# Kernel tuning notes

Measured on AMD Instinct MI355X. Metric: run time of the kernel, lower is better.

Reference implementation:

```python
import jax, jax.numpy as jnp
import numpy as np

N, P, F_, E, G = 2048, 256, 512, 32768, 64  # nodes, points/node, feat_len, edges, graphs
H, D = 8, 64  # GATv2 heads, per-head dim (feat_len // 8)


def _w(k, shape, fan):
    return jax.random.normal(k, shape, jnp.float32) / np.sqrt(fan)


def setup_inputs():
    ks = jax.random.split(jax.random.key(0), 40)
    inp = {
        'pcd': jax.random.normal(ks[0], (N, P, 3), jnp.float32),
        'volume': jax.random.uniform(ks[1], (N,), jnp.float32),
        'distance': jax.random.uniform(ks[2], (N,), jnp.float32),
        'edge_count': jax.random.uniform(ks[3], (N,), jnp.float32),
        'y': (jax.random.uniform(ks[4], (N,), jnp.float32) < 0.05).astype(jnp.float32),
        # PointNet (1x1 convs == per-point matmuls, no bias)
        'pn_w1': _w(ks[5], (3, 64), 3), 'pn_w2': _w(ks[6], (64, 64), 64),
        'pn_w3': _w(ks[7], (64, 64), 64), 'pn_w4': _w(ks[8], (64, 128), 64),
        'pn_w5': _w(ks[9], (128, F_), 128),
        # MLPMultiFeature
        'mf_w1': _w(ks[10], (3, F_), 3), 'mf_b1': jnp.zeros((F_,), jnp.float32),
        'mf_w2': _w(ks[11], (2 * F_, F_), 2 * F_), 'mf_b2': jnp.zeros((F_,), jnp.float32),
        # GATv2 layer 1
        'g1_wl': _w(ks[12], (F_, F_), F_), 'g1_bl': jnp.zeros((F_,), jnp.float32),
        'g1_wr': _w(ks[13], (F_, F_), F_), 'g1_br': jnp.zeros((F_,), jnp.float32),
        'g1_att': _w(ks[14], (H, D), D), 'g1_bias': jnp.zeros((F_,), jnp.float32),
        # GATv2 layer 2
        'g2_wl': _w(ks[15], (F_, F_), F_), 'g2_bl': jnp.zeros((F_,), jnp.float32),
        'g2_wr': _w(ks[16], (F_, F_), F_), 'g2_br': jnp.zeros((F_,), jnp.float32),
        'g2_att': _w(ks[17], (H, D), D), 'g2_bias': jnp.zeros((F_,), jnp.float32),
        # classifier
        'cl_w1': _w(ks[18], (F_, 64), F_), 'cl_b1': jnp.zeros((64,), jnp.float32),
        'cl_w2': _w(ks[19], (64, 64), 64), 'cl_b2': jnp.zeros((64,), jnp.float32),
        'cl_w3': _w(ks[20], (64, 1), 64), 'cl_b3': jnp.zeros((1,), jnp.float32),
        'edge_index': jax.random.randint(ks[21], (2, E), 0, N),
        'num_graphs': G,
    }
    return inp


def _gatv2(x, src, dst, wl, bl, wr, br, att, bias, n):
    h, d = att.shape
    xl = (x @ wl + bl).reshape(n, h, d)  # source transform
    xr = (x @ wr + br).reshape(n, h, d)  # target transform
    e = jax.nn.leaky_relu(xl[src] + xr[dst], 0.2)          # [E', H, D]
    score = jnp.einsum('ehd,hd->eh', e, att)               # [E', H]
    m = jax.ops.segment_max(score, dst, num_segments=n)
    m = jnp.where(jnp.isfinite(m), m, 0.0)
    p = jnp.exp(score - m[dst])
    denom = jax.ops.segment_sum(p, dst, num_segments=n)
    alpha = p / denom[dst]                                  # segment softmax over in-edges
    out = jax.ops.segment_sum(alpha[:, :, None] * xl[src], dst, num_segments=n)
    return out.reshape(n, h * d) + bias


def _forward(pcd, volume, distance, edge_count, y,
             pn_w1, pn_w2, pn_w3, pn_w4, pn_w5,
             mf_w1, mf_b1, mf_w2, mf_b2,
             g1_wl, g1_bl, g1_wr, g1_br, g1_att, g1_bias,
             g2_wl, g2_bl, g2_wr, g2_br, g2_att, g2_bias,
             cl_w1, cl_b1, cl_w2, cl_b2, cl_w3, cl_b3,
             edge_index, num_graphs):
    n = pcd.shape[0]
    # PointNet: 1x1 convs (BN=Identity) then global max-pool over points
    hdd = jax.nn.relu(pcd @ pn_w1)
    hdd = jax.nn.relu(hdd @ pn_w2)
    hdd = jax.nn.relu(hdd @ pn_w3)
    hdd = jax.nn.relu(hdd @ pn_w4)
    hdd = jax.nn.relu(hdd @ pn_w5)
    pc_feat = hdd.max(axis=1)  # [N, F]
    # multi-feature MLP
    vd = jnp.stack([volume, distance, edge_count], axis=1)
    vdf = jax.nn.relu(vd @ mf_w1 + mf_b1)
    x = jax.nn.relu(jnp.concatenate([pc_feat, vdf], axis=1) @ mf_w2 + mf_b2)
    # GAT (GATv2Conv adds self-loops by default)
    loop = jnp.arange(n)
    src = jnp.concatenate([edge_index[0], loop])
    dst = jnp.concatenate([edge_index[1], loop])
    x = jax.nn.relu(_gatv2(x, src, dst, g1_wl, g1_bl, g1_wr, g1_br, g1_att, g1_bias, n))
    x = _gatv2(x, src, dst, g2_wl, g2_bl, g2_wr, g2_br, g2_att, g2_bias, n)
    # classifier
    hc = jax.nn.relu(x @ cl_w1 + cl_b1)
    hc = jax.nn.relu(hc @ cl_w2 + cl_b2)
    logits = (hc @ cl_w3 + cl_b3)[:, 0]
    # BCEWithLogitsLoss (mean)
    loss = jnp.mean(jnp.maximum(logits, 0.0) - logits * y + jnp.log1p(jnp.exp(-jnp.abs(logits))))
    # per-graph top1-hit; graphs are contiguous & equal-size, and the torch
    # slice logits[mask_min:mask_max] excludes the segment's last node -> [:, :-1]
    npg = n // num_graphs
    lg = logits.reshape(num_graphs, npg)[:, :-1]
    yg = y.reshape(num_graphs, npg)[:, :-1]
    hits = (jnp.argmax(lg, axis=1) == jnp.argmax(yg, axis=1)).astype(jnp.float32)
    return loss, jnp.mean(hits)


def reference(pcd, volume, distance, edge_count, y,
              pn_w1, pn_w2, pn_w3, pn_w4, pn_w5,
              mf_w1, mf_b1, mf_w2, mf_b2,
              g1_wl, g1_bl, g1_wr, g1_br, g1_att, g1_bias,
              g2_wl, g2_bl, g2_wr, g2_br, g2_att, g2_bias,
              cl_w1, cl_b1, cl_w2, cl_b2, cl_w3, cl_b3,
              edge_index, num_graphs):
    return _forward(pcd, volume, distance, edge_count, y,
                    pn_w1, pn_w2, pn_w3, pn_w4, pn_w5,
                    mf_w1, mf_b1, mf_w2, mf_b2,
                    g1_wl, g1_bl, g1_wr, g1_br, g1_att, g1_bias,
                    g2_wl, g2_bl, g2_wr, g2_br, g2_att, g2_bias,
                    cl_w1, cl_b1, cl_w2, cl_b2, cl_w3, cl_b3,
                    edge_index, num_graphs)
```

## Files before the change

### kernel.cpp

```cpp
#include <hip/hip_runtime.h>
#include <cstdint>
#include <cstddef>

#define N_NODES 2048
#define N_PTS 256
#define N_EDGE 32768
#define N_EDGE_TOT (N_EDGE + N_NODES)
#define NPG 32

typedef __attribute__((ext_vector_type(8))) short bfx8;
typedef __attribute__((ext_vector_type(4))) float f32x4;
typedef unsigned short ushort_t;

#define MFMA16(a, b, c) __builtin_amdgcn_mfma_f32_16x16x32_bf16(a, b, c, 0, 0, 0)

__device__ inline int e_src(const int* ei, int e) { return e < N_EDGE ? ei[e] : e - N_EDGE; }
__device__ inline int e_dst(const int* ei, int e) { return e < N_EDGE ? ei[N_EDGE + e] : e - N_EDGE; }

__device__ inline ushort_t bf16_rtne(float v) {
  unsigned u = __float_as_uint(v);
  return (ushort_t)((u + 0x7fffu + ((u >> 16) & 1u)) >> 16);
}
__device__ inline void split2(float v, ushort_t& h, ushort_t& l) {
  h = bf16_rtne(v);
  float hf = __uint_as_float(((unsigned)h) << 16);
  l = bf16_rtne(v - hf);
}

__device__ inline unsigned cvtpk_bf16(float a, float b) {
  unsigned r;
  asm("v_cvt_pk_bf16_f32 %0, %1, %2" : "=v"(r) : "v"(a), "v"(b));
  return r;
}
__device__ inline void split2pk(float a, float b, unsigned& hp, unsigned& lp) {
  hp = cvtpk_bf16(a, b);
  float ha = __uint_as_float(hp << 16);
  float hb = __uint_as_float(hp & 0xffff0000u);
  lp = cvtpk_bf16(a - ha, b - hb);
}

__global__ void k_hist(const int* __restrict__ ei, int* __restrict__ cnt) {
  int e = blockIdx.x * 256 + threadIdx.x;
  if (e >= N_EDGE_TOT) return;
  atomicAdd(&cnt[e_dst(ei, e)], 1);
}

__global__ __launch_bounds__(256) void k_scan(int* __restrict__ cnt, int* __restrict__ row_ptr) {
  __shared__ int sS[256];
  const int t = threadIdx.x;
  int v[8]; int s = 0;
#pragma unroll
  for (int i = 0; i < 8; i++) { v[i] = cnt[t * 8 + i]; s += v[i]; }
#pragma unroll
  for (int i = 0; i < 8; i++) cnt[t * 8 + i] = 0;
  sS[t] = s;
  __syncthreads();
  for (int off = 1; off < 256; off <<= 1) {
    int x = 0;
    if (t >= off) x = sS[t - off];
    __syncthreads();
    sS[t] += x;
    __syncthreads();
  }
  int run = sS[t] - s;
#pragma unroll
  for (int i = 0; i < 8; i++) { row_ptr[t * 8 + i] = run; run += v[i]; }
  if (t == 255) row_ptr[2048] = run;
}

__global__ void k_scatter(const int* __restrict__ ei, const int* __restrict__ row_ptr,
                          int* __restrict__ cur, int* __restrict__ edge_list) {
  int e = blockIdx.x * 256 + threadIdx.x;
  if (e >= N_EDGE_TOT) return;
  int d = e_dst(ei, e);
  int pos = row_ptr[d] + atomicAdd(&cur[d], 1);
  edge_list[pos] = e;
}

__device__ inline void split_tile(const float* __restrict__ src, ushort_t* __restrict__ dh,
                                  ushort_t* __restrict__ dl, int K, int N,
                                  int k0, int n0, int t) {
  __shared__ float sT[64][65];
  const int lr = t >> 4, lc = (t & 15) * 4;
#pragma unroll
  for (int p = 0; p < 4; p++) {
    int k = lr + p * 16;
    float4 v = *(const float4*)(src + (size_t)(k0 + k) * N + n0 + lc);
    sT[k][lc] = v.x; sT[k][lc + 1] = v.y; sT[k][lc + 2] = v.z; sT[k][lc + 3] = v.w;
  }
  __syncthreads();
  const int wr = t >> 4, wc = (t & 15) * 4;
#pragma unroll
  for (int p = 0; p < 4; p++) {
    int nrow = wr + p * 16;
    uint2 uh, ul;
    split2pk(sT[wc + 0][nrow], sT[wc + 1][nrow], uh.x, ul.x);
    split2pk(sT[wc + 2][nrow], sT[wc + 3][nrow], uh.y, ul.y);
    *(uint2*)(dh + (size_t)(n0 + nrow) * K + k0 + wc) = uh;
    *(uint2*)(dl + (size_t)(n0 + nrow) * K + k0 + wc) = ul;
  }
}

__global__ __launch_bounds__(256) void k_split(const float* __restrict__ src,
                                               ushort_t* __restrict__ dh,
                                               ushort_t* __restrict__ dl, int K, int N) {
  split_tile(src, dh, dl, K, N, blockIdx.x * 64, blockIdx.y * 64, threadIdx.x);
}

__global__ __launch_bounds__(256) void k_split4(const float* __restrict__ s0,
                                                const float* __restrict__ s1,
                                                const float* __restrict__ s2,
                                                const float* __restrict__ s3,
                                                ushort_t* __restrict__ base) {
  const int z = blockIdx.z;
  const float* src = (z == 0) ? s0 : (z == 1) ? s1 : (z == 2) ? s2 : s3;
  ushort_t* dh = base + (size_t)(z >> 1) * 1048576 + (size_t)(z & 1) * 262144;
  ushort_t* dl = dh + 524288;
  split_tile(src, dh, dl, 512, 512, blockIdx.x * 64, blockIdx.y * 64, threadIdx.x);
}

constexpr size_t U_W2H = 0,       U_W2L = 4096;
constexpr size_t U_W3H = 8192,    U_W3L = 12288;
constexpr size_t U_W4H = 16384,   U_W4L = 24576;
constexpr size_t U_W5H = 32768,   U_W5L = 98304;
constexpr size_t U_MFH = 163840,  U_MFL = 688128;
constexpr size_t U_G1H = 1212416;
constexpr size_t U_G1L = 1736704;
constexpr size_t U_G2H = 2260992;
constexpr size_t U_G2L = 2785280;
constexpr size_t U_CL1H = 3309568, U_CL1L = 3342336;
constexpr size_t U_END  = 3375104;

__global__ __launch_bounds__(256) void k_splitPN(const float* __restrict__ w2,
                                                 const float* __restrict__ w3,
                                                 const float* __restrict__ w4,
                                                 const float* __restrict__ w5,
                                                 ushort_t* __restrict__ ush) {
  const int z = blockIdx.x;
  const float* src; ushort_t* dh; ushort_t* dl; int K, N, k0, n0;
  if (z == 0)      { src = w2; dh = ush + U_W2H; dl = ush + U_W2L; K = 64;  N = 64;  k0 = 0; n0 = 0; }
  else if (z == 1) { src = w3; dh = ush + U_W3H; dl = ush + U_W3L; K = 64;  N = 64;  k0 = 0; n0 = 0; }
  else if (z < 4)  { src = w4; dh = ush + U_W4H; dl = ush + U_W4L; K = 64;  N = 128; k0 = 0; n0 = (z - 2) * 64; }
  else { int i = z - 4; src = w5; dh = ush + U_W5H; dl = ush + U_W5L; K = 128; N = 512;
         k0 = (i >> 3) * 64; n0 = (i & 7) * 64; }
  split_tile(src, dh, dl, K, N, k0, n0, threadIdx.x);
}

__global__ __launch_bounds__(512, 2) void k_pointnet(
    const float* __restrict__ pcd, const float* __restrict__ w1,
    const ushort_t* __restrict__ w2th, const ushort_t* __restrict__ w2tl,
    const ushort_t* __restrict__ w3th, const ushort_t* __restrict__ w3tl,
    const ushort_t* __restrict__ w4th, const ushort_t* __restrict__ w4tl,
    const ushort_t* __restrict__ w5th, const ushort_t* __restrict__ w5tl,
    float* __restrict__ xcat) {
  __shared__ ushort_t sH4H[256 * 128];
  __shared__ ushort_t sH4L[256 * 128];
  __shared__ ushort_t sBAH[32 * 64];
  __shared__ ushort_t sBAL[32 * 64];
  __shared__ ushort_t sBBH[32 * 64];
  __shared__ ushort_t sBBL[32 * 64];
  __shared__ float sP[256 * 3];
  __shared__ float sW1[3 * 64];

  char* H4H = (char*)sH4H; char* H4L = (char*)sH4L;
  char* BAH = (char*)sBAH; char* BAL = (char*)sBAL;
  char* BBH = (char*)sBBH; char* BBL = (char*)sBBL;

  const int t = threadIdx.x;
  const int node = blockIdx.x;
  const int w = t >> 6;
  const int lane = t & 63;
  const int l15 = lane & 15;
  const int kg = lane >> 4;

  for (int i = t; i < 768; i += 512) sP[i] = pcd[(size_t)node * 768 + i];
  for (int i = t; i < 192; i += 512) sW1[i] = w1[i];

  const int rt14 = w >> 2;
  const int ct14 = w & 3;
  bfx8 b2h[2], b2l[2], b3h[2], b3l[2], b4h[2][2], b4l[2][2];
#pragma unroll
  for (int ks = 0; ks < 2; ks++) {
    {
      int col = ct14 * 16 + l15;
      int k = ks * 32 + kg * 8;
      b2h[ks] = *(const bfx8*)(w2th + col * 64 + k);
      b2l[ks] = *(const bfx8*)(w2tl + col * 64 + k);
      b3h[ks] = *(const bfx8*)(w3th + col * 64 + k);
      b3l[ks] = *(const bfx8*)(w3tl + col * 64 + k);
    }
#pragma unroll
    for (int u = 0; u < 2; u++) {
      int col = (ct14 * 2 + u) * 16 + l15;
      int k = ks * 32 + kg * 8;
      b4h[u][ks] = *(const bfx8*)(w4th + col * 64 + k);
      b4l[u][ks] = *(const bfx8*)(w4tl + col * 64 + k);
    }
  }
  __syncthreads();

  const int l1r = t >> 4, l1c = t & 15;

  {
    const float* p = &sP[(0 * 32 + l1r) * 3];
    float p0 = p[0], p1 = p[1], p2 = p[2];
    float vv[4];
#pragma unroll
    for (int j = 0; j < 4; j++) {
      int col = l1c * 4 + j;
      vv[j] = fmaxf(fmaf(p0, sW1[col], fmaf(p1, sW1[64 + col], p2 * sW1[128 + col])), 0.0f);
    }
    unsigned hp0, lp0, hp1, lp1;
    split2pk(vv[0], vv[1], hp0, lp0);
    split2pk(vv[2], vv[3], hp1, lp1);
    int off = (l1r * 128 + l1c * 8) ^ ((l1r & 7) << 4);
    *(unsigned*)(BAH + off) = hp0;
    *(unsigned*)(BAH + off + 4) = hp1;
    *(unsigned*)(BAL + off) = lp0;
    *(unsigned*)(BAL + off + 4) = lp1;
  }
  __syncthreads();

  for (int c = 0; c < 8; c++) {
    char* Ah = (c & 1) ? BBH : BAH;
    char* Al = (c & 1) ? BBL : BAL;
    char* Bh = (c & 1) ? BAH : BBH;
    char* Bl = (c & 1) ? BAL : BBL;
    {
      f32x4 acc = {0.f, 0.f, 0.f, 0.f};
#pragma unroll
      for (int ks = 0; ks < 2; ks++) {
        int row = rt14 * 16 + l15;
        int k0 = ks * 32 + kg * 8;
        int offb = (row * 128 + k0 * 2) ^ ((row & 7) << 4);
        bfx8 ah = *(const bfx8*)(Ah + offb);
        bfx8 al = *(const bfx8*)(Al + offb);
        acc = MFMA16(ah, b2h[ks], acc);
        acc = MFMA16(al, b2h[ks], acc);
        acc = MFMA16(ah, b2l[ks], acc);
      }
      unsigned hp[2], lp[2];
      split2pk(fmaxf(acc[0], 0.f), fmaxf(acc[1], 0.f), hp[0], lp[0]);
      split2pk(fmaxf(acc[2], 0.f), fmaxf(acc[3], 0.f), hp[1], lp[1]);
      const int colb = (ct14 * 16 + l15) * 2;
      const int rowb = rt14 * 16 + kg * 4;
#pragma unroll
      for (int j = 0; j < 4; j++) {
        int row = rowb + j;
        int off = (row * 128 + colb) ^ ((row & 7) << 4);
        *(ushort_t*)(Bh + off) = (ushort_t)(hp[j >> 1] >> ((j & 1) * 16));
        *(ushort_t*)(Bl + off) = (ushort_t)(lp[j >> 1] >> ((j & 1) * 16));
      }
    }
    __syncthreads();
    {
      f32x4 acc = {0.f, 0.f, 0.f, 0.f};
#pragma unroll
      for (int ks = 0; ks < 2; ks++) {
        int row = rt14 * 16 + l15;
        int k0 = ks * 32 + kg * 8;
        int offb = (row * 128 + k0 * 2) ^ ((row & 7) << 4);
        bfx8 ah = *(const bfx8*)(Bh + offb);
        bfx8 al = *(const bfx8*)(Bl + offb);
        acc = MFMA16(ah, b3h[ks], acc);
        acc = MFMA16(al, b3h[ks], acc);
        acc = MFMA16(ah, b3l[ks], acc);
      }
      unsigned hp[2], lp[2];
      split2pk(fmaxf(acc[0], 0.f), fmaxf(acc[1], 0.f), hp[0], lp[0]);
      split2pk(fmaxf(acc[2], 0.f), fmaxf(acc[3], 0.f), hp[1], lp[1]);
      const int colb = (ct14 * 16 + l15) * 2;
      const int rowb = rt14 * 16 + kg * 4;
#pragma unroll
      for (int j = 0; j < 4; j++) {
        int row = rowb + j;
        int off = (row * 128 + colb) ^ ((row & 7) << 4);
        *(ushort_t*)(Ah + off) = (ushort_t)(hp[j >> 1] >> ((j & 1) * 16));
        *(ushort_t*)(Al + off) = (ushort_t)(lp[j >> 1] >> ((j & 1) * 16));
      }
    }
    __syncthreads();
    {
      f32x4 acc[2];
      acc[0] = (f32x4){0.f, 0.f, 0.f, 0.f};
      acc[1] = (f32x4){0.f, 0.f, 0.f, 0.f};
#pragma unroll
      for (int ks = 0; ks < 2; ks++) {
        int row = rt14 * 16 + l15;
        int k0 = ks * 32 + kg * 8;
        int offb = (row * 128 + k0 * 2) ^ ((row & 7) << 4);
        bfx8 ah = *(const bfx8*)(Ah + offb);
        bfx8 al = *(const bfx8*)(Al + offb);
#pragma unroll
        for (int u = 0; u < 2; u++) {
          acc[u] = MFMA16(ah, b4h[u][ks], acc[u]);
          acc[u] = MFMA16(al, b4h[u][ks], acc[u]);
          acc[u] = MFMA16(ah, b4l[u][ks], acc[u]);
        }
      }
      if (c < 7) {
        const float* p = &sP[((c + 1) * 32 + l1r) * 3];
        float p0 = p[0], p1 = p[1], p2 = p[2];
        float vv[4];
#pragma unroll
        for (int j = 0; j < 4; j++) {
          int col = l1c * 4 + j;
          vv[j] = fmaxf(fmaf(p0, sW1[col], fmaf(p1, sW1[64 + col], p2 * sW1[128 + col])), 0.0f);
        }
        unsigned hp0, lp0, hp1, lp1;
        split2pk(vv[0], vv[1], hp0, lp0);
        split2pk(vv[2], vv[3], hp1, lp1);
        int off = (l1r * 128 + l1c * 8) ^ ((l1r & 7) << 4);
        *(unsigned*)(Bh + off) = hp0;
        *(unsigned*)(Bh + off + 4) = hp1;
        *(unsigned*)(Bl + off) = lp0;
        *(unsigned*)(Bl + off + 4) = lp1;
      }
#pragma unroll
      for (int j = 0; j < 4; j++) {
        unsigned hp, lp;
        split2pk(fmaxf(acc[0][j], 0.f), fmaxf(acc[1][j], 0.f), hp, lp);
        int row = c * 32 + rt14 * 16 + kg * 4 + j;
        int col0 = (ct14 * 2) * 16 + l15;
        int off0 = (row * 256 + col0 * 2) ^ ((row & 7) << 4);
        int off1 = ((row * 256 + (col0 + 16) * 2)) ^ ((row & 7) << 4);
        *(ushort_t*)(H4H + off0) = (ushort_t)hp;
        *(ushort_t*)(H4H + off1) = (ushort_t)(hp >> 16);
        *(ushort_t*)(H4L + off0) = (ushort_t)lp;
        *(ushort_t*)(H4L + off1) = (ushort_t)(lp >> 16);
      }
    }
    __syncthreads();
  }

  __builtin_amdgcn_sched_barrier(0);
  bfx8 b5h[4][4], b5l[4][4];
  const int c0 = w * 64;
#pragma unroll
  for (int ks = 0; ks < 4; ks++)
#pragma unroll
    for (int ct = 0; ct < 4; ct++) {
      int col = c0 + ct * 16 + l15;
      int k = ks * 32 + kg * 8;
      b5h[ks][ct] = *(const bfx8*)(w5th + col * 128 + k);
      b5l[ks][ct] = *(const bfx8*)(w5tl + col * 128 + k);
    }
  float runmax[4] = {0.f, 0.f, 0.f, 0.f};
  for (int rc = 0; rc < 8; rc++) {
    f32x4 acc[2][4];
#pragma unroll
    for (int rt = 0; rt < 2; rt++)
#pragma unroll
      for (int ct = 0; ct < 4; ct++) acc[rt][ct] = (f32x4){0.f, 0.f, 0.f, 0.f};
#pragma unroll
    for (int ks = 0; ks < 4; ks++) {
      bfx8 ah[2], al[2];
#pragma unroll
      for (int rt = 0; rt < 2; rt++) {
        int row = rc * 32 + rt * 16 + l15;
        int k0 = ks * 32 + kg * 8;
        int off = (row * 256 + k0 * 2) ^ ((row & 7) << 4);
        ah[rt] = *(const bfx8*)(H4H + off);
        al[rt] = *(const bfx8*)(H4L + off);
      }
#pragma unroll
      for (int ct = 0; ct < 4; ct++)
#pragma unroll
        for (int rt = 0; rt < 2; rt++) {
          acc[rt][ct] = MFMA16(ah[rt], b5h[ks][ct], acc[rt][ct]);
          acc[rt][ct] = MFMA16(al[rt], b5h[ks][ct], acc[rt][ct]);
          acc[rt][ct] = MFMA16(ah[rt], b5l[ks][ct], acc[rt][ct]);
        }
    }
#pragma unroll
    for (int ct = 0; ct < 4; ct++)
#pragma unroll
      for (int rt = 0; rt < 2; rt++)
#pragma unroll
        for (int j = 0; j < 4; j++)
          runmax[ct] = fmaxf(runmax[ct], acc[rt][ct][j]);
  }
#pragma unroll
  for (int ct = 0; ct < 4; ct++) {
    float m = runmax[ct];
    m = fmaxf(m, __shfl_xor(m, 16));
    m = fmaxf(m, __shfl_xor(m, 32));
    if (lane < 16) xcat[(size_t)node * 1024 + c0 + ct * 16 + lane] = m;
  }
}

__global__ void k_vdf(const float* __restrict__ vol, const float* __restrict__ dist,
                      const float* __restrict__ ec, const float* __restrict__ w1,
                      const float* __restrict__ b1, float* __restrict__ xcat) {
  int idx = blockIdx.x * 256 + threadIdx.x;
  int n = idx >> 9, j = idx & 511;
  float v = vol[n] * w1[j] + dist[n] * w1[512 + j] + ec[n] * w1[1024 + j] + b1[j];
  xcat[(size_t)n * 1024 + 512 + j] = fmaxf(v, 0.0f);
}

template <int ACT>
__global__ __launch_bounds__(256) void k_mgemm(const float* __restrict__ A,
                                               const ushort_t* __restrict__ Bh,
                                               const ushort_t* __restrict__ Bl,
                                               const float* __restrict__ bias,
                                               const float* __restrict__ bias2,
                                               float* __restrict__ C,
                                               int M, int N, int K) {
  __shared__ ushort_t sAh[4096], sAl[4096], sBh[4096], sBl[4096];
  char* pAh = (char*)sAh; char* pAl = (char*)sAl;
  char* pBh = (char*)sBh; char* pBl = (char*)sBl;
  const int t = threadIdx.x;
  const int w = t >> 6, lane = t & 63, l15 = lane & 15, kg = lane >> 4;
  const int row0 = blockIdx.x * 64, col0 = blockIdx.y * 64;
  const int sr = t >> 2;
  const int sc = (t & 3) * 16;
  const int sswz = (sr & 7) << 4;
  const int sbase = sr * 128 + sc * 2;
  f32x4 acc[4];
#pragma unroll
  for (int ct = 0; ct < 4; ct++) acc[ct] = (f32x4){0.f, 0.f, 0.f, 0.f};

  for (int kb = 0; kb < K; kb += 64) {
    __syncthreads();
    {
      const float* Ap = A + (size_t)(row0 + sr) * K + kb + sc;
      float4 a0 = *(const float4*)(Ap);
      float4 a1 = *(const float4*)(Ap + 4);
      float4 a2 = *(const float4*)(Ap + 8);
      float4 a3 = *(const float4*)(Ap + 12);
      union { bfx8 v; unsigned u[4]; } vh0, vh1, vl0, vl1;
      split2pk(a0.x, a0.y, vh0.u[0], vl0.u[0]);
      split2pk(a0.z, a0.w, vh0.u[1], vl0.u[1]);
      split2pk(a1.x, a1.y, vh0.u[2], vl0.u[2]);
      split2pk(a1.z, a1.w, vh0.u[3], vl0.u[3]);
      split2pk(a2.x, a2.y, vh1.u[0], vl1.u[0]);
      split2pk(a2.z, a2.w, vh1.u[1], vl1.u[1]);
      split2pk(a3.x, a3.y, vh1.u[2], vl1.u[2]);
      split2pk(a3.z, a3.w, vh1.u[3], vl1.u[3]);
      *(bfx8*)(pAh + ((sbase) ^ sswz)) = vh0.v;
      *(bfx8*)(pAh + ((sbase + 16) ^ sswz)) = vh1.v;
      *(bfx8*)(pAl + ((sbase) ^ sswz)) = vl0.v;
      *(bfx8*)(pAl + ((sbase + 16) ^ sswz)) = vl1.v;
    }
    {
      const ushort_t* Bph = Bh + (size_t)(col0 + sr) * K + kb + sc;
      const ushort_t* Bpl = Bl + (size_t)(col0 + sr) * K + kb + sc;
      bfx8 b0 = *(const bfx8*)Bph, b1 = *(const bfx8*)(Bph + 8);
      bfx8 c0v = *(const bfx8*)Bpl, c1v = *(const bfx8*)(Bpl + 8);
      *(bfx8*)(pBh + ((sbase) ^ sswz)) = b0;
      *(bfx8*)(pBh + ((sbase + 16) ^ sswz)) = b1;
      *(bfx8*)(pBl + ((sbase) ^ sswz)) = c0v;
      *(bfx8*)(pBl + ((sbase + 16) ^ sswz)) = c1v;
    }
    __syncthreads();
#pragma unroll
    for (int ks = 0; ks < 2; ks++) {
      const int arow = w * 16 + l15;
      const int k2 = (ks * 32 + kg * 8) * 2;
      const int aoff = (arow * 128 + k2) ^ ((arow & 7) << 4);
      bfx8 ah = *(const bfx8*)(pAh + aoff);
      bfx8 al = *(const bfx8*)(pAl + aoff);
#pragma unroll
      for (int ct = 0; ct < 4; ct++) {
        const int bcol = ct * 16 + l15;
        const int boff = (bcol * 128 + k2) ^ ((bcol & 7) << 4);
        bfx8 bh = *(const bfx8*)(pBh + boff);
        bfx8 bl = *(const bfx8*)(pBl + boff);
        acc[ct] = MFMA16(ah, bh, acc[ct]);
        acc[ct] = MFMA16(al, bh, acc[ct]);
        acc[ct] = MFMA16(ah, bl, acc[ct]);
      }
    }
  }
#pragma unroll
  for (int ct = 0; ct < 4; ct++)
#pragma unroll
    for (int j = 0; j < 4; j++) {
      int r = row0 + w * 16 + kg * 4 + j;
      int cc = col0 + ct * 16 + l15;
      float b = (cc < 512) ? bias[cc] : bias2[cc - 512];
      float v = acc[ct][j] + b;
      if (ACT == 1) v = fmaxf(v, 0.0f);
      C[(size_t)r * N + cc] = v;
    }
}

__global__ __launch_bounds__(256) void k_mgemm_mf(const float* __restrict__ A,
                                                  const float* __restrict__ vol,
                                                  const float* __restrict__ dist,
                                                  const float* __restrict__ ec,
                                                  const float* __restrict__ w1,
                                                  const float* __restrict__ b1,
                                                  const ushort_t* __restrict__ Bh,
                                                  const ushort_t* __restrict__ Bl,
                                                  const float* __restrict__ bias,
                                                  float* __restrict__ C) {
  const int M = 2048, N = 512, K = 1024;
  __shared__ ushort_t sAh[4096], sAl[4096], sBh[4096], sBl[4096];
  char* pAh = (char*)sAh; char* pAl = (char*)sAl;
  char* pBh = (char*)sBh; char* pBl = (char*)sBl;
  const int t = threadIdx.x;
  const int w = t >> 6, lane = t & 63, l15 = lane & 15, kg = lane >> 4;
  const int row0 = blockIdx.x * 64, col0 = blockIdx.y * 64;
  const int sr = t >> 2;
  const int sc = (t & 3) * 16;
  const int sswz = (sr & 7) << 4;
  const int sbase = sr * 128 + sc * 2;
  f32x4 acc[4];
#pragma unroll
  for (int ct = 0; ct < 4; ct++) acc[ct] = (f32x4){0.f, 0.f, 0.f, 0.f};

  const int r = row0 + sr;
  const float v0 = vol[r], d0 = dist[r], e0 = ec[r];

  for (int kb = 0; kb < K; kb += 64) {
    __syncthreads();
    {
      const int kc = kb + sc;
      float4 a0, a1, a2, a3;
      if (kc < 512) {
        const float* Ap = A + (size_t)r * 1024 + kc;
        a0 = *(const float4*)(Ap);
        a1 = *(const float4*)(Ap + 4);
        a2 = *(const float4*)(Ap + 8);
        a3 = *(const float4*)(Ap + 12);
      } else {
        const int j = kc - 512;
        float tmp[16];
#pragma unroll
        for (int i = 0; i < 16; i++) {
          float v = v0 * w1[j + i] + d0 * w1[512 + j + i] + e0 * w1[1024 + j + i] + b1[j + i];
          tmp[i] = fmaxf(v, 0.0f);
        }
        a0 = make_float4(tmp[0], tmp[1], tmp[2], tmp[3]);
        a1 = make_float4(tmp[4], tmp[5], tmp[6], tmp[7]);
        a2 = make_float4(tmp[8], tmp[9], tmp[10], tmp[11]);
        a3 = make_float4(tmp[12], tmp[13], tmp[14], tmp[15]);
      }
      union { bfx8 v; unsigned u[4]; } vh0, vh1, vl0, vl1;
      split2pk(a0.x, a0.y, vh0.u[0], vl0.u[0]);
      split2pk(a0.z, a0.w, vh0.u[1], vl0.u[1]);
      split2pk(a1.x, a1.y, vh0.u[2], vl0.u[2]);
      split2pk(a1.z, a1.w, vh0.u[3], vl0.u[3]);
      split2pk(a2.x, a2.y, vh1.u[0], vl1.u[0]);
      split2pk(a2.z, a2.w, vh1.u[1], vl1.u[1]);
      split2pk(a3.x, a3.y, vh1.u[2], vl1.u[2]);
      split2pk(a3.z, a3.w, vh1.u[3], vl1.u[3]);
      *(bfx8*)(pAh + ((sbase) ^ sswz)) = vh0.v;
      *(bfx8*)(pAh + ((sbase + 16) ^ sswz)) = vh1.v;
      *(bfx8*)(pAl + ((sbase) ^ sswz)) = vl0.v;
      *(bfx8*)(pAl + ((sbase + 16) ^ sswz)) = vl1.v;
    }
    {
      const ushort_t* Bph = Bh + (size_t)(col0 + sr) * K + kb + sc;
      const ushort_t* Bpl = Bl + (size_t)(col0 + sr) * K + kb + sc;
      bfx8 b0 = *(const bfx8*)Bph, b1v = *(const bfx8*)(Bph + 8);
      bfx8 c0v = *(const bfx8*)Bpl, c1v = *(const bfx8*)(Bpl + 8);
      *(bfx8*)(pBh + ((sbase) ^ sswz)) = b0;
      *(bfx8*)(pBh + ((sbase + 16) ^ sswz)) = b1v;
      *(bfx8*)(pBl + ((sbase) ^ sswz)) = c0v;
      *(bfx8*)(pBl + ((sbase + 16) ^ sswz)) = c1v;
    }
    __syncthreads();
#pragma unroll
    for (int ks = 0; ks < 2; ks++) {
      const int arow = w * 16 + l15;
      const int k2 = (ks * 32 + kg * 8) * 2;
      const int aoff = (arow * 128 + k2) ^ ((arow & 7) << 4);
      bfx8 ah = *(const bfx8*)(pAh + aoff);
      bfx8 al = *(const bfx8*)(pAl + aoff);
#pragma unroll
      for (int ct = 0; ct < 4; ct++) {
        const int bcol = ct * 16 + l15;
        const int boff = (bcol * 128 + k2) ^ ((bcol & 7) << 4);
        bfx8 bh = *(const bfx8*)(pBh + boff);
        bfx8 bl = *(const bfx8*)(pBl + boff);
        acc[ct] = MFMA16(ah, bh, acc[ct]);
        acc[ct] = MFMA16(al, bh, acc[ct]);
        acc[ct] = MFMA16(ah, bl, acc[ct]);
      }
    }
  }
#pragma unroll
  for (int ct = 0; ct < 4; ct++)
#pragma unroll
    for (int j = 0; j < 4; j++) {
      int rr = row0 + w * 16 + kg * 4 + j;
      int cc = col0 + ct * 16 + l15;
      float v = acc[ct][j] + bias[cc];
      C[(size_t)rr * N + cc] = fmaxf(v, 0.0f);
    }
}

template <int ACT>
__global__ __launch_bounds__(256) void k_gemm(const float* __restrict__ A,
                                              const float* __restrict__ W,
                                              const float* __restrict__ bias,
                                              float* __restrict__ C, int M, int N, int K,
                                              int ldc, int cof) {
  __shared__ float sA[64][17];
  __shared__ float sW[16][64];
  const int t = threadIdx.x;
  const int row0 = blockIdx.x * 64, col0 = blockIdx.y * 64;
  const int tr = t >> 4, tc = t & 15;
  const int la_r = t >> 2, la_c = (t & 3) * 4;
  const int lw_r = t >> 4, lw_c = (t & 15) * 4;
  float acc[4][4] = {};
  for (int kb = 0; kb < K; kb += 16) {
    __syncthreads();
    float4 av = *(const float4*)(A + (size_t)(row0 + la_r) * K + kb + la_c);
    sA[la_r][la_c + 0] = av.x; sA[la_r][la_c + 1] = av.y;
    sA[la_r][la_c + 2] = av.z; sA[la_r][la_c + 3] = av.w;
    float4 wv = *(const float4*)(W + (size_t)(kb + lw_r) * N + col0 + lw_c);
    *(float4*)&sW[lw_r][lw_c] = wv;
    __syncthreads();
#pragma unroll
    for (int kk = 0; kk < 16; kk++) {
      float a0 = sA[tr * 4 + 0][kk], a1 = sA[tr * 4 + 1][kk];
      float a2 = sA[tr * 4 + 2][kk], a3 = sA[tr * 4 + 3][kk];
      float4 w4 = *(const float4*)&sW[kk][tc * 4];
      acc[0][0] = fmaf(a0, w4.x, acc[0][0]); acc[0][1] = fmaf(a0, w4.y, acc[0][1]);
      acc[0][2] = fmaf(a0, w4.z, acc[0][2]); acc[0][3] = fmaf(a0, w4.w, acc[0][3]);
      acc[1][0] = fmaf(a1, w4.x, acc[1][0]); acc[1][1] = fmaf(a1, w4.y, acc[1][1]);
      acc[1][2] = fmaf(a1, w4.z, acc[1][2]); acc[1][3] = fmaf(a1, w4.w, acc[1][3]);
      acc[2][0] = fmaf(a2, w4.x, acc[2][0]); acc[2][1] = fmaf(a2, w4.y, acc[2][1]);
      acc[2][2] = fmaf(a2, w4.z, acc[2][2]); acc[2][3] = fmaf(a2, w4.w, acc[2][3]);
      acc[3][0] = fmaf(a3, w4.x, acc[3][0]); acc[3][1] = fmaf(a3, w4.y, acc[3][1]);
      acc[3][2] = fmaf(a3, w4.z, acc[3][2]); acc[3][3] = fmaf(a3, w4.w, acc[3][3]);
    }
  }
#pragma unroll
  for (int i = 0; i < 4; i++) {
    int r = row0 + tr * 4 + i;
#pragma unroll
    for (int j = 0; j < 4; j++) {
      int c = col0 + tc * 4 + j;
      float v = acc[i][j] + bias[c];
      if (ACT == 1) v = fmaxf(v, 0.0f);
      C[(size_t)r * ldc + cof + c] = v;
    }
  }
}

template <int ACT>
__global__ __launch_bounds__(256) void k_gat(
    const float* __restrict__ xlr, const float* __restrict__ att,
    const int* __restrict__ row_ptr, const int* __restrict__ edge_list,
    const int* __restrict__ ei, const float* __restrict__ bias,
    float* __restrict__ out) {
  __shared__ float sXr[512];
  __shared__ float sPb[32][8];
  __shared__ int sSrc[32];
  __shared__ float sM[8], sD[8], sScale[8];
  const int n = blockIdx.x, t = threadIdx.x;
  const int wv = t >> 6, l = t & 63;
  float attr[8];
#pragma unroll
  for (int h = 0; h < 8; h++) attr[h] = att[h * 64 + l];
  for (int i = t; i < 512; i += 256) sXr[i] = xlr[(size_t)n * 1024 + 512 + i];
  if (t < 8) { sM[t] = -1e30f; sD[t] = 0.f; }
  const int f0 = t, f1 = t + 256;
  const int h0 = f0 >> 6, h1 = f1 >> 6;
  float acc0 = 0.f, acc1 = 0.f;
  const int beg = row_ptr[n], end = row_ptr[n + 1];
  __syncthreads();
  for (int b = beg; b < end; b += 32) {
    const int cnt = min(32, end - b);
    for (int i = wv; i < cnt; i += 4) {
      const int e = edge_list[b + i];
      const int s = e_src(ei, e);
      const float* xs = xlr + (size_t)s * 1024;
      float ps[8];
#pragma unroll
      for (int h = 0; h < 8; h++) {
        float v = xs[h * 64 + l] + sXr[h * 64 + l];
        v = v > 0.f ? v : 0.2f * v;
        ps[h] = v * attr[h];
      }
#pragma unroll
      for (int off = 1; off < 64; off <<= 1)
#pragma unroll
        for (int h = 0; h < 8; h++) ps[h] += __shfl_xor(ps[h], off);
      if (l == 0) {
        sSrc[i] = s;
#pragma unroll
        for (int h = 0; h < 8; h++) sPb[i][h] = ps[h];
      }
    }
    __syncthreads();
    if (t < 8) {
      float m = sM[t];
      for (int i = 0; i < cnt; i++) m = fmaxf(m, sPb[i][t]);
      float scale = expf(sM[t] - m);
      float d = sD[t] * scale;
      for (int i = 0; i < cnt; i++) {
        float p = expf(sPb[i][t] - m);
        sPb[i][t] = p;
        d += p;
      }
      sM[t] = m; sD[t] = d; sScale[t] = scale;
    }
    __syncthreads();
    acc0 *= sScale[h0];
    acc1 *= sScale[h1];
    for (int i = 0; i < cnt; i++) {
      const float* xs = xlr + (size_t)sSrc[i] * 1024;
      acc0 = fmaf(sPb[i][h0], xs[f0], acc0);
      acc1 = fmaf(sPb[i][h1], xs[f1], acc1);
    }
    __syncthreads();
  }
  float v0 = acc0 / sD[h0] + bias[f0];
  float v1 = acc1 / sD[h1] + bias[f1];
  if (ACT == 1) { v0 = fmaxf(v0, 0.f); v1 = fmaxf(v1, 0.f); }
  out[(size_t)n * 512 + f0] = v0;
  out[(size_t)n * 512 + f1] = v1;
}

__global__ __launch_bounds__(1024) void k_final(const float* __restrict__ hc2,
                                                const float* __restrict__ w3,
                                                const float* __restrict__ b3,
                                                const float* __restrict__ y,
                                                float* __restrict__ out) {
  __shared__ float sL[2048];
  __shared__ float sRed[1024];
  __shared__ float sW[64];
  const int t = threadIdx.x;
  if (t < 64) sW[t] = w3[t];
  __syncthreads();
  float lp = 0.0f;
  for (int n = t; n < 2048; n += 1024) {
    const float4* r = (const float4*)(hc2 + (size_t)n * 64);
    float a = 0.0f;
#pragma unroll
    for (int k = 0; k < 16; k++) {
      float4 v = r[k];
      a += v.x * sW[4 * k] + v.y * sW[4 * k + 1] + v.z * sW[4 * k + 2] + v.w * sW[4 * k + 3];
    }
    a += b3[0];
    sL[n] = a;
    lp += fmaxf(a, 0.0f) - a * y[n] + log1pf(expf(-fabsf(a)));
  }
  sRed[t] = lp;
  __syncthreads();
  for (int off = 512; off > 0; off >>= 1) {
    if (t < off) sRed[t] += sRed[t + off];
    __syncthreads();
  }
  if (t == 0) out[0] = sRed[0] * (1.0f / 2048.0f);
  __syncthreads();
  float hit = 0.0f;
  if (t < 64) {
    const int base = t * NPG;
    float bl = sL[base]; int bi = 0;
    float by = y[base];  int byi = 0;
    for (int i = 1; i < NPG - 1; i++) {
      float v = sL[base + i];
      if (v > bl) { bl = v; bi = i; }
      float w = y[base + i];
      if (w > by) { by = w; byi = i; }
    }
    hit = (bi == byi) ? 1.0f : 0.0f;
  }
  __syncthreads();
  sRed[t] = hit;
  __syncthreads();
  for (int off = 512; off > 0; off >>= 1) {
    if (t < off) sRed[t] += sRed[t + off];
    __syncthreads();
  }
  if (t == 0) out[1] = sRed[0] * (1.0f / 64.0f);
}

constexpr size_t OFF_XCAT = 0;
constexpr size_t OFF_X1   = OFF_XCAT + (size_t)2048 * 1024;
constexpr size_t OFF_XL   = OFF_X1 + (size_t)2048 * 512;
constexpr size_t OFF_XR   = OFF_XL + (size_t)2048 * 512;
constexpr size_t OFF_G1   = OFF_XR + (size_t)2048 * 512;
constexpr size_t OFF_G2   = OFF_G1 + (size_t)2048 * 512;
constexpr size_t OFF_HC1  = OFF_G2 + (size_t)2048 * 512;
constexpr size_t OFF_HC2  = OFF_HC1 + (size_t)2048 * 64;
constexpr size_t OFF_SC   = OFF_HC2 + (size_t)2048 * 64;
constexpr size_t OFF_P    = OFF_SC + (size_t)N_EDGE_TOT * 8;
constexpr size_t OFF_M    = OFF_P + (size_t)N_EDGE_TOT * 8;
constexpr size_t OFF_DEN  = OFF_M + (size_t)2048 * 8;
constexpr size_t OFF_RP   = OFF_DEN + (size_t)2048 * 8;
constexpr size_t OFF_CNT  = OFF_RP + 2052;
constexpr size_t OFF_EL   = OFF_CNT + 2048;
constexpr size_t OFF_USH  = OFF_EL + 34816;

constexpr size_t WS_NEED_FULL = (OFF_USH + (U_END + 1) / 2) * sizeof(float);

extern "C" void kernel_launch(void* const* d_in, const int* in_sizes, int n_in,
                              void* d_out, int out_size, void* d_ws, size_t ws_size,
                              hipStream_t stream) {
  const float* pcd   = (const float*)d_in[0];
  const float* vol   = (const float*)d_in[1];
  const float* dist  = (const float*)d_in[2];
  const float* ecnt  = (const float*)d_in[3];
  const float* y     = (const float*)d_in[4];
  const float* pn_w1 = (const float*)d_in[5];
  const float* pn_w2 = (const float*)d_in[6];
  const float* pn_w3 = (const float*)d_in[7];
  const float* pn_w4 = (const float*)d_in[8];
  const float* pn_w5 = (const float*)d_in[9];
  const float* mf_w1 = (const float*)d_in[10];
  const float* mf_b1 = (const float*)d_in[11];
  const float* mf_w2 = (const float*)d_in[12];
  const float* mf_b2 = (const float*)d_in[13];
  const float* g1_wl = (const float*)d_in[14];
  const float* g1_bl = (const float*)d_in[15];
  const float* g1_wr = (const float*)d_in[16];
  const float* g1_br = (const float*)d_in[17];
  const float* g1_at = (const float*)d_in[18];
  const float* g1_bi = (const float*)d_in[19];
  const float* g2_wl = (const float*)d_in[20];
  const float* g2_bl = (const float*)d_in[21];
  const float* g2_wr = (const float*)d_in[22];
  const float* g2_br = (const float*)d_in[23];
  const float* g2_at = (const float*)d_in[24];
  const float* g2_bi = (const float*)d_in[25];
  const float* cl_w1 = (const float*)d_in[26];
  const float* cl_b1 = (const float*)d_in[27];
  const float* cl_w2 = (const float*)d_in[28];
  const float* cl_b2 = (const float*)d_in[29];
  const float* cl_w3 = (const float*)d_in[30];
  const float* cl_b3 = (const float*)d_in[31];
  const int*   ei    = (const int*)d_in[32];
  float* out = (float*)d_out;
  float* ws  = (float*)d_ws;

  float* xcat = ws + OFF_XCAT;
  float* x1   = ws + OFF_X1;
  float* g1o  = ws + OFF_G1;
  float* g2o  = ws + OFF_G2;
  float* hc1  = ws + OFF_HC1;
  float* hc2  = ws + OFF_HC2;
  int* rp     = (int*)(ws + OFF_RP);
  int* cnt    = (int*)(ws + OFF_CNT);
  int* el     = (int*)(ws + OFF_EL);
  ushort_t* ush = (ushort_t*)(ws + OFF_USH);

  const bool full = (ws_size >= WS_NEED_FULL);

  hipMemsetAsync(cnt, 0, 2048 * sizeof(int), stream);
  k_hist<<<(N_EDGE_TOT + 255) / 256, 256, 0, stream>>>(ei, cnt);
  k_scan<<<1, 256, 0, stream>>>(cnt, rp);
  k_scatter<<<(N_EDGE_TOT + 255) / 256, 256, 0, stream>>>(ei, rp, cnt, el);

  k_splitPN<<<20, 256, 0, stream>>>(pn_w2, pn_w3, pn_w4, pn_w5, ush);
  if (full) {
    k_split<<<dim3(16, 8), 256, 0, stream>>>(mf_w2, ush + U_MFH, ush + U_MFL, 1024, 512);
    k_split4<<<dim3(8, 8, 4), 256, 0, stream>>>(g1_wl, g1_wr, g2_wl, g2_wr, ush + U_G1H);
    k_split<<<dim3(8, 1), 256, 0, stream>>>(cl_w1, ush + U_CL1H, ush + U_CL1L, 512, 64);
  }

  k_pointnet<<<N_NODES, 512, 0, stream>>>(pcd, pn_w1,
      ush + U_W2H, ush + U_W2L, ush + U_W3H, ush + U_W3L,
      ush + U_W4H, ush + U_W4L, ush + U_W5H, ush + U_W5L, xcat);
  if (full) {
    k_mgemm_mf<<<dim3(32, 8), 256, 0, stream>>>(xcat, vol, dist, ecnt, mf_w1, mf_b1,
                                                ush + U_MFH, ush + U_MFL, mf_b2, x1);
  } else {
    k_vdf<<<2048 * 512 / 256, 256, 0, stream>>>(vol, dist, ecnt, mf_w1, mf_b1, xcat);
    k_gemm<1><<<dim3(32, 8), 256, 0, stream>>>(xcat, mf_w2, mf_b2, x1, 2048, 512, 1024, 512, 0);
  }

  if (full) {
    k_mgemm<0><<<dim3(32, 16), 256, 0, stream>>>(x1, ush + U_G1H, ush + U_G1L, g1_bl, g1_br, xcat, 2048, 1024, 512);
    k_gat<1><<<N_NODES, 256, 0, stream>>>(xcat, g1_at, rp, el, ei, g1_bi, g1o);
    k_mgemm<0><<<dim3(32, 16), 256, 0, stream>>>(g1o, ush + U_G2H, ush + U_G2L, g2_bl, g2_br, xcat, 2048, 1024, 512);
    k_gat<0><<<N_NODES, 256, 0, stream>>>(xcat, g2_at, rp, el, ei, g2_bi, g2o);
    k_mgemm<1><<<dim3(32, 1), 256, 0, stream>>>(g2o, ush + U_CL1H, ush + U_CL1L, cl_b1, cl_b1, hc1, 2048, 64, 512);
  } else {
    k_gemm<0><<<dim3(32, 8), 256, 0, stream>>>(x1, g1_wl, g1_bl, xcat, 2048, 512, 512, 1024, 0);
    k_gemm<0><<<dim3(32, 8), 256, 0, stream>>>(x1, g1_wr, g1_br, xcat, 2048, 512, 512, 1024, 512);
    k_gat<1><<<N_NODES, 256, 0, stream>>>(xcat, g1_at, rp, el, ei, g1_bi, g1o);
    k_gemm<0><<<dim3(32, 8), 256, 0, stream>>>(g1o, g2_wl, g2_bl, xcat, 2048, 512, 512, 1024, 0);
    k_gemm<0><<<dim3(32, 8), 256, 0, stream>>>(g1o, g2_wr, g2_br, xcat, 2048, 512, 512, 1024, 512);
    k_gat<0><<<N_NODES, 256, 0, stream>>>(xcat, g2_at, rp, el, ei, g2_bi, g2o);
    k_gemm<1><<<dim3(32, 1), 256, 0, stream>>>(g2o, cl_w1, cl_b1, hc1, 2048, 64, 512, 64, 0);
  }
  k_gemm<1><<<dim3(32, 1), 256, 0, stream>>>(hc1, cl_w2, cl_b2, hc2, 2048, 64, 64, 64, 0);
  k_final<<<1, 1024, 0, stream>>>(hc2, cl_w3, cl_b3, y, out);
}
```

Baseline: 439.4 us.

## Merge weight-split kernels into one launch and widen GATv2 GEMM tiles

Four weight-splitting kernels are folded into a single 412-block launch to cut launch overhead. The two GATv2 projection GEMMs move to a new kernel with 64x128 output tiles, where each wave computes a 32x64 sub-tile. A and B fragments are reused across more MFMAs, halving the grid and the redundant A loads and splits. The larger B shared tile raises LDS use per block, which may lower occupancy.

Result: no change. 443.0 us (+0.8%).

```diff
diff --git a/kernel.cpp b/kernel.cpp
--- a/kernel.cpp
+++ b/kernel.cpp
@@ -16,16 +16,6 @@
 
 __device__ inline int e_src(const int* ei, int e) { return e < N_EDGE ? ei[e] : e - N_EDGE; }
 __device__ inline int e_dst(const int* ei, int e) { return e < N_EDGE ? ei[N_EDGE + e] : e - N_EDGE; }
-
-__device__ inline ushort_t bf16_rtne(float v) {
-  unsigned u = __float_as_uint(v);
-  return (ushort_t)((u + 0x7fffu + ((u >> 16) & 1u)) >> 16);
-}
-__device__ inline void split2(float v, ushort_t& h, ushort_t& l) {
-  h = bf16_rtne(v);
-  float hf = __uint_as_float(((unsigned)h) << 16);
-  l = bf16_rtne(v - hf);
-}
 
 __device__ inline unsigned cvtpk_bf16(float a, float b) {
   unsigned r;
@@ -99,24 +89,6 @@
     *(uint2*)(dh + (size_t)(n0 + nrow) * K + k0 + wc) = uh;
     *(uint2*)(dl + (size_t)(n0 + nrow) * K + k0 + wc) = ul;
   }
-}
-
-__global__ __launch_bounds__(256) void k_split(const float* __restrict__ src,
-                                               ushort_t* __restrict__ dh,
-                                               ushort_t* __restrict__ dl, int K, int N) {
-  split_tile(src, dh, dl, K, N, blockIdx.x * 64, blockIdx.y * 64, threadIdx.x);
-}
-
-__global__ __launch_bounds__(256) void k_split4(const float* __restrict__ s0,
-                                                const float* __restrict__ s1,
-                                                const float* __restrict__ s2,
-                                                const float* __restrict__ s3,
-                                                ushort_t* __restrict__ base) {
-  const int z = blockIdx.z;
-  const float* src = (z == 0) ? s0 : (z == 1) ? s1 : (z == 2) ? s2 : s3;
-  ushort_t* dh = base + (size_t)(z >> 1) * 1048576 + (size_t)(z & 1) * 262144;
-  ushort_t* dl = dh + 524288;
-  split_tile(src, dh, dl, 512, 512, blockIdx.x * 64, blockIdx.y * 64, threadIdx.x);
 }
 
 constexpr size_t U_W2H = 0,       U_W2L = 4096;
@@ -131,19 +103,39 @@
 constexpr size_t U_CL1H = 3309568, U_CL1L = 3342336;
 constexpr size_t U_END  = 3375104;
 
-__global__ __launch_bounds__(256) void k_splitPN(const float* __restrict__ w2,
-                                                 const float* __restrict__ w3,
-                                                 const float* __restrict__ w4,
-                                                 const float* __restrict__ w5,
-                                                 ushort_t* __restrict__ ush) {
+__global__ __launch_bounds__(256) void k_split_all(
+    const float* __restrict__ w2, const float* __restrict__ w3,
+    const float* __restrict__ w4, const float* __restrict__ w5,
+    const float* __restrict__ mfw, const float* __restrict__ g1l,
+    const float* __restrict__ g1r, const float* __restrict__ g2l,
+    const float* __restrict__ g2r, const float* __restrict__ clw,
+    ushort_t* __restrict__ ush, int full) {
   const int z = blockIdx.x;
-  const float* src; ushort_t* dh; ushort_t* dl; int K, N, k0, n0;
-  if (z == 0)      { src = w2; dh = ush + U_W2H; dl = ush + U_W2L; K = 64;  N = 64;  k0 = 0; n0 = 0; }
-  else if (z == 1) { src = w3; dh = ush + U_W3H; dl = ush + U_W3L; K = 64;  N = 64;  k0 = 0; n0 = 0; }
-  else if (z < 4)  { src = w4; dh = ush + U_W4H; dl = ush + U_W4L; K = 64;  N = 128; k0 = 0; n0 = (z - 2) * 64; }
-  else { int i = z - 4; src = w5; dh = ush + U_W5H; dl = ush + U_W5L; K = 128; N = 512;
-         k0 = (i >> 3) * 64; n0 = (i & 7) * 64; }
-  split_tile(src, dh, dl, K, N, k0, n0, threadIdx.x);
+  const int t = threadIdx.x;
+  if (z < 20) {
+    const float* src; ushort_t* dh; ushort_t* dl; int K, N, k0, n0;
+    if (z == 0)      { src = w2; dh = ush + U_W2H; dl = ush + U_W2L; K = 64;  N = 64;  k0 = 0; n0 = 0; }
+    else if (z == 1) { src = w3; dh = ush + U_W3H; dl = ush + U_W3L; K = 64;  N = 64;  k0 = 0; n0 = 0; }
+    else if (z < 4)  { src = w4; dh = ush + U_W4H; dl = ush + U_W4L; K = 64;  N = 128; k0 = 0; n0 = (z - 2) * 64; }
+    else { int i = z - 4; src = w5; dh = ush + U_W5H; dl = ush + U_W5L; K = 128; N = 512;
+           k0 = (i >> 3) * 64; n0 = (i & 7) * 64; }
+    split_tile(src, dh, dl, K, N, k0, n0, t);
+  } else if (!full) {
+    return;
+  } else if (z < 148) {
+    int i = z - 20;
+    split_tile(mfw, ush + U_MFH, ush + U_MFL, 1024, 512, (i >> 3) * 64, (i & 7) * 64, t);
+  } else if (z < 404) {
+    int i = z - 148;
+    int m = i >> 6, tile = i & 63;
+    const float* src = (m == 0) ? g1l : (m == 1) ? g1r : (m == 2) ? g2l : g2r;
+    ushort_t* dh = ush + U_G1H + (size_t)(m >> 1) * 1048576 + (size_t)(m & 1) * 262144;
+    ushort_t* dl = dh + 524288;
+    split_tile(src, dh, dl, 512, 512, (tile >> 3) * 64, (tile & 7) * 64, t);
+  } else {
+    int i = z - 404;
+    split_tile(clw, ush + U_CL1H, ush + U_CL1L, 512, 64, i * 64, 0, t);
+  }
 }
 
 __global__ __launch_bounds__(512, 2) void k_pointnet(
@@ -483,6 +475,106 @@
       if (ACT == 1) v = fmaxf(v, 0.0f);
       C[(size_t)r * N + cc] = v;
     }
+}
+
+__global__ __launch_bounds__(256) void k_mgemm2(const float* __restrict__ A,
+                                                const ushort_t* __restrict__ Bh,
+                                                const ushort_t* __restrict__ Bl,
+                                                const float* __restrict__ bias,
+                                                const float* __restrict__ bias2,
+                                                float* __restrict__ C,
+                                                int M, int N, int K) {
+  __shared__ ushort_t sAh[4096], sAl[4096];
+  __shared__ ushort_t sBh[8192], sBl[8192];
+  char* pAh = (char*)sAh; char* pAl = (char*)sAl;
+  char* pBh = (char*)sBh; char* pBl = (char*)sBl;
+  const int t = threadIdx.x;
+  const int w = t >> 6, lane = t & 63, l15 = lane & 15, kg = lane >> 4;
+  const int rgrp = w >> 1, cgrp = w & 1;
+  const int row0 = blockIdx.x * 64, col0 = blockIdx.y * 128;
+  const int sr = t >> 2, sc = (t & 3) * 16;
+  const int sswz = (sr & 7) << 4;
+  const int sbase = sr * 128 + sc * 2;
+  const int bcolS = t & 127, bkS = (t >> 7) * 32;
+  f32x4 acc[2][4];
+#pragma unroll
+  for (int rt = 0; rt < 2; rt++)
+#pragma unroll
+    for (int ct = 0; ct < 4; ct++) acc[rt][ct] = (f32x4){0.f, 0.f, 0.f, 0.f};
+
+  for (int kb = 0; kb < K; kb += 64) {
+    __syncthreads();
+    {
+      const float* Ap = A + (size_t)(row0 + sr) * K + kb + sc;
+      float4 a0 = *(const float4*)(Ap);
+      float4 a1 = *(const float4*)(Ap + 4);
+      float4 a2 = *(const float4*)(Ap + 8);
+      float4 a3 = *(const float4*)(Ap + 12);
+      union { bfx8 v; unsigned u[4]; } vh0, vh1, vl0, vl1;
+      split2pk(a0.x, a0.y, vh0.u[0], vl0.u[0]);
+      split2pk(a0.z, a0.w, vh0.u[1], vl0.u[1]);
+      split2pk(a1.x, a1.y, vh0.u[2], vl0.u[2]);
+      split2pk(a1.z, a1.w, vh0.u[3], vl0.u[3]);
+      split2pk(a2.x, a2.y, vh1.u[0], vl1.u[0]);
+      split2pk(a2.z, a2.w, vh1.u[1], vl1.u[1]);
+      split2pk(a3.x, a3.y, vh1.u[2], vl1.u[2]);
+      split2pk(a3.z, a3.w, vh1.u[3], vl1.u[3]);
+      *(bfx8*)(pAh + ((sbase) ^ sswz)) = vh0.v;
+      *(bfx8*)(pAh + ((sbase + 16) ^ sswz)) = vh1.v;
+      *(bfx8*)(pAl + ((sbase) ^ sswz)) = vl0.v;
+      *(bfx8*)(pAl + ((sbase + 16) ^ sswz)) = vl1.v;
+    }
+    {
+      const ushort_t* Bph = Bh + (size_t)(col0 + bcolS) * K + kb + bkS;
+      const ushort_t* Bpl = Bl + (size_t)(col0 + bcolS) * K + kb + bkS;
+      const int bswz = (bcolS & 7) << 4;
+      const int bbase = bcolS * 128 + bkS * 2;
+#pragma unroll
+      for (int q = 0; q < 4; q++) {
+        bfx8 bh = *(const bfx8*)(Bph + q * 8);
+        bfx8 bl = *(const bfx8*)(Bpl + q * 8);
+        *(bfx8*)(pBh + ((bbase + q * 16) ^ bswz)) = bh;
+        *(bfx8*)(pBl + ((bbase + q * 16) ^ bswz)) = bl;
+      }
+    }
+    __syncthreads();
+#pragma unroll
+    for (int ks = 0; ks < 2; ks++) {
+      const int k2 = (ks * 32 + kg * 8) * 2;
+      bfx8 ah[2], al[2];
+#pragma unroll
+      for (int rt = 0; rt < 2; rt++) {
+        const int arow = rgrp * 32 + rt * 16 + l15;
+        const int aoff = (arow * 128 + k2) ^ ((arow & 7) << 4);
+        ah[rt] = *(const bfx8*)(pAh + aoff);
+        al[rt] = *(const bfx8*)(pAl + aoff);
+      }
+#pragma unroll
+      for (int ct = 0; ct < 4; ct++) {
+        const int bcol = cgrp * 64 + ct * 16 + l15;
+        const int boff = (bcol * 128 + k2) ^ ((bcol & 7) << 4);
+        bfx8 bh = *(const bfx8*)(pBh + boff);
+        bfx8 bl = *(const bfx8*)(pBl + boff);
+#pragma unroll
+        for (int rt = 0; rt < 2; rt++) {
+          acc[rt][ct] = MFMA16(ah[rt], bh, acc[rt][ct]);
+          acc[rt][ct] = MFMA16(al[rt], bh, acc[rt][ct]);
+          acc[rt][ct] = MFMA16(ah[rt], bl, acc[rt][ct]);
+        }
+      }
+    }
+  }
+#pragma unroll
+  for (int rt = 0; rt < 2; rt++)
+#pragma unroll
+    for (int ct = 0; ct < 4; ct++)
+#pragma unroll
+      for (int j = 0; j < 4; j++) {
+        int r = row0 + rgrp * 32 + rt * 16 + kg * 4 + j;
+        int cc = col0 + cgrp * 64 + ct * 16 + l15;
+        float b = (cc < 512) ? bias[cc] : bias2[cc - 512];
+        C[(size_t)r * N + cc] = acc[rt][ct][j] + b;
+      }
 }
 
 __global__ __launch_bounds__(256) void k_mgemm_mf(const float* __restrict__ A,
@@ -848,12 +940,9 @@
   k_scan<<<1, 256, 0, stream>>>(cnt, rp);
   k_scatter<<<(N_EDGE_TOT + 255) / 256, 256, 0, stream>>>(ei, rp, cnt, el);
 
-  k_splitPN<<<20, 256, 0, stream>>>(pn_w2, pn_w3, pn_w4, pn_w5, ush);
-  if (full) {
-    k_split<<<dim3(16, 8), 256, 0, stream>>>(mf_w2, ush + U_MFH, ush + U_MFL, 1024, 512);
-    k_split4<<<dim3(8, 8, 4), 256, 0, stream>>>(g1_wl, g1_wr, g2_wl, g2_wr, ush + U_G1H);
-    k_split<<<dim3(8, 1), 256, 0, stream>>>(cl_w1, ush + U_CL1H, ush + U_CL1L, 512, 64);
-  }
+  k_split_all<<<412, 256, 0, stream>>>(pn_w2, pn_w3, pn_w4, pn_w5, mf_w2,
+                                       g1_wl, g1_wr, g2_wl, g2_wr, cl_w1,
+                                       ush, full ? 1 : 0);
 
   k_pointnet<<<N_NODES, 512, 0, stream>>>(pcd, pn_w1,
       ush + U_W2H, ush + U_W2L, ush + U_W3H, ush + U_W3L,
@@ -867,9 +956,9 @@
   }
 
   if (full) {
-    k_mgemm<0><<<dim3(32, 16), 256, 0, stream>>>(x1, ush + U_G1H, ush + U_G1L, g1_bl, g1_br, xcat, 2048, 1024, 512);
+    k_mgemm2<<<dim3(32, 8), 256, 0, stream>>>(x1, ush + U_G1H, ush + U_G1L, g1_bl, g1_br, xcat, 2048, 1024, 512);
     k_gat<1><<<N_NODES, 256, 0, stream>>>(xcat, g1_at, rp, el, ei, g1_bi, g1o);
-    k_mgemm<0><<<dim3(32, 16), 256, 0, stream>>>(g1o, ush + U_G2H, ush + U_G2L, g2_bl, g2_br, xcat, 2048, 1024, 512);
+    k_mgemm2<<<dim3(32, 8), 256, 0, stream>>>(g1o, ush + U_G2H, ush + U_G2L, g2_bl, g2_br, xcat, 2048, 1024, 512);
     k_gat<0><<<N_NODES, 256, 0, stream>>>(xcat, g2_at, rp, el, ei, g2_bi, g2o);
     k_mgemm<1><<<dim3(32, 1), 256, 0, stream>>>(g2o, ush + U_CL1H, ush + U_CL1L, cl_b1, cl_b1, hc1, 2048, 64, 512);
   } else {
```
